# Kernel optimization log

Measured on AMD Instinct MI355X. Metric: run time of the kernel, lower is better.

The kernel has to match this reference:

```python
import jax, jax.numpy as jnp
from jax import lax
import numpy as np

B, CIN, HC, K, REC = 64, 64, 64, 3, 5
MG = 240 // REC  # 48
EPS = 1e-8


def conv2d(x, w, b, pad):
    y = lax.conv_general_dilated(x, w, (1, 1), [(pad, pad), (pad, pad)],
                                 dimension_numbers=('NCHW', 'OIHW', 'NCHW'))
    return y + b[None, :, None, None]


def conv_transpose2d(x, w, b, stride, pad):
    # PyTorch ConvTranspose2d: w is (Cin, Cout, kH, kW)
    k = w.shape[2]
    w_t = jnp.transpose(w[:, :, ::-1, ::-1], (1, 0, 2, 3))  # -> OIHW, flipped
    y = lax.conv_general_dilated(x, w_t, (1, 1),
                                 [(k - 1 - pad, k - 1 - pad)] * 2,
                                 lhs_dilation=(stride, stride),
                                 dimension_numbers=('NCHW', 'OIHW', 'NCHW'))
    return y + b[None, :, None, None]


def leaky(x):
    return jnp.where(x >= 0, x, 0.2 * x)


def setup_inputs() -> dict:
    key = jax.random.key(0)
    ks = jax.random.split(key, 12)
    s = 0.05
    return {
        'x': jax.random.normal(ks[0], (B, CIN, 64, 64), jnp.float32),
        'h': jax.random.normal(ks[1], (B, HC, 64, 64), jnp.float32),
        'c': jax.random.normal(ks[2], (B, HC, 64, 64), jnp.float32),
        'recalled_memory_feature': jax.random.normal(ks[3], (B, REC, MG, 32, 32), jnp.float32),
        'conv_w': jax.random.normal(ks[4], (5 * HC, CIN + HC, K, K), jnp.float32) * s,
        'conv_b': jax.random.normal(ks[5], (5 * HC,), jnp.float32) * s,
        'convc_w': jax.random.normal(ks[6], (MG, HC, 1, 1), jnp.float32) * s,
        'convc_b': jax.random.normal(ks[7], (MG,), jnp.float32) * s,
        'convssm_w': jax.random.normal(ks[8], (MG, MG, 4, 4), jnp.float32) * s,
        'convssm_b': jax.random.normal(ks[9], (MG,), jnp.float32) * s,
        'convfuse_w': jax.random.normal(ks[10], (HC, MG + HC, 1, 1), jnp.float32) * s,
        'convfuse_b': jax.random.normal(ks[11], (HC,), jnp.float32) * s,
    }


def reference(x, h, c, recalled_memory_feature, conv_w, conv_b, convc_w, convc_b,
              convssm_w, convssm_b, convfuse_w, convfuse_b):
    rm = recalled_memory_feature.reshape(B, REC, MG, 32, 32)
    rm_avg = rm.mean(axis=(3, 4))                      # (B, REC, MG)
    q = leaky(conv2d(c, convc_w, convc_b, 0))          # (B, MG, 64, 64)
    q_avg = q.mean(axis=(2, 3))                        # (B, MG)
    # cosine similarity along channel dim, vectorized over (B, REC)
    qn = jnp.maximum(jnp.linalg.norm(q_avg, axis=1, keepdims=True), EPS)   # (B,1)
    mn = jnp.maximum(jnp.linalg.norm(rm_avg, axis=2), EPS)                  # (B,REC)
    cos = jnp.einsum('bm,brm->br', q_avg, rm_avg) / (qn * mn)               # (B,REC)
    attn = jax.nn.softmax(cos, axis=1)                                      # (B,REC)
    mt = jnp.einsum('br,brmhw->bmhw', attn, rm)        # (B, MG, 32, 32)
    mt = leaky(conv_transpose2d(mt, convssm_w, convssm_b, 2, 1))  # (B, MG, 64, 64)

    gates = conv2d(jnp.concatenate((x, h), axis=1), conv_w, conv_b, K // 2)
    i, f, g, o, lam = jnp.split(gates, 5, axis=1)
    i = jax.nn.sigmoid(i)
    f = jax.nn.sigmoid(f)
    o = jax.nn.sigmoid(o)
    g = jnp.tanh(g)
    lam = jax.nn.sigmoid(lam)
    c_new = f * c + i * g
    h_new = o * jnp.tanh(conv2d(jnp.concatenate((c_new, mt), axis=1), convfuse_w, convfuse_b, 0))
    h_out = lam * h_new + (1.0 - lam) * h
    return (h_out, c_new)
```

## Files before the change

### kernel.cpp

```cpp
#include <hip/hip_runtime.h>
#include <hip/hip_bf16.h>
#include <cstdint>

#define HW 4096
#define MGc 48
#define RECc 5

typedef __attribute__((ext_vector_type(8))) short bf16x8;
typedef __attribute__((ext_vector_type(4))) float f32x4;

__device__ __forceinline__ float sigf(float x) { return 1.f / (1.f + expf(-x)); }
__device__ __forceinline__ float leakyf(float x) { return x >= 0.f ? x : 0.2f * x; }
__device__ __forceinline__ unsigned short f2bfu(float f) {
  __hip_bfloat16 b = __float2bfloat16(f);
  return *reinterpret_cast<unsigned short*>(&b);
}
__device__ __forceinline__ void gload_lds16(const void* g, void* l) {
  __builtin_amdgcn_global_load_lds(
      (const __attribute__((address_space(1))) unsigned int*)g,
      (__attribute__((address_space(3))) unsigned int*)l, 16, 0, 0);
}

__global__ __launch_bounds__(256) void k_rm_sum(const float* __restrict__ rm,
                                                float* __restrict__ rm_sum) {
  int row = blockIdx.x;
  const float4* p = reinterpret_cast<const float4*>(rm + (size_t)row * 1024);
  float4 v = p[threadIdx.x];
  float s = v.x + v.y + v.z + v.w;
  #pragma unroll
  for (int off = 32; off; off >>= 1) s += __shfl_down(s, off);
  __shared__ float sred[4];
  if ((threadIdx.x & 63) == 0) sred[threadIdx.x >> 6] = s;
  __syncthreads();
  if (threadIdx.x == 0) rm_sum[row] = sred[0] + sred[1] + sred[2] + sred[3];
}

__global__ __launch_bounds__(256) void k_q_part(const float* __restrict__ c,
    const float* __restrict__ ccw, const float* __restrict__ ccb,
    float* __restrict__ q_part) {
  __shared__ float wl[MGc * 64];
  __shared__ float bl[MGc];
  __shared__ float red[4][MGc];
  int b = blockIdx.y, seg = blockIdx.x;
  for (int i = threadIdx.x; i < MGc * 64; i += 256) wl[i] = ccw[i];
  if (threadIdx.x < MGc) bl[threadIdx.x] = ccb[threadIdx.x];
  __syncthreads();
  int px = seg * 256 + threadIdx.x;
  float acc[MGc];
  #pragma unroll
  for (int m = 0; m < MGc; m++) acc[m] = 0.f;
  const float* cp = c + (size_t)b * 64 * HW + px;
  for (int ci = 0; ci < 64; ci++) {
    float v = cp[(size_t)ci * HW];
    #pragma unroll
    for (int m = 0; m < MGc; m++) acc[m] += wl[m * 64 + ci] * v;
  }
  int lane = threadIdx.x & 63, wv = threadIdx.x >> 6;
  #pragma unroll
  for (int m = 0; m < MGc; m++) {
    float t = leakyf(acc[m] + bl[m]);
    #pragma unroll
    for (int off = 32; off; off >>= 1) t += __shfl_down(t, off);
    if (lane == 0) red[wv][m] = t;
  }
  __syncthreads();
  if (threadIdx.x < MGc) {
    float t = red[0][threadIdx.x] + red[1][threadIdx.x] + red[2][threadIdx.x] + red[3][threadIdx.x];
    q_part[((size_t)b * 16 + seg) * MGc + threadIdx.x] = t;
  }
}

__global__ __launch_bounds__(64) void k_attn(const float* __restrict__ rm_sum,
    const float* __restrict__ q_part, float* __restrict__ attn) {
  int b = blockIdx.x, lane = threadIdx.x;
  float q = 0.f;
  if (lane < MGc) {
    float s = 0.f;
    for (int sg = 0; sg < 16; sg++) s += q_part[((size_t)b * 16 + sg) * MGc + lane];
    q = s * (1.f / 4096.f);
  }
  float qs = q * q;
  #pragma unroll
  for (int off = 32; off; off >>= 1) qs += __shfl_xor(qs, off);
  float qn = fmaxf(sqrtf(qs), 1e-8f);
  float cosv[RECc];
  #pragma unroll
  for (int r = 0; r < RECc; r++) {
    float m = 0.f;
    if (lane < MGc) m = rm_sum[((size_t)b * RECc + r) * MGc + lane] * (1.f / 1024.f);
    float d = q * m, ms = m * m;
    #pragma unroll
    for (int off = 32; off; off >>= 1) { d += __shfl_xor(d, off); ms += __shfl_xor(ms, off); }
    float mn = fmaxf(sqrtf(ms), 1e-8f);
    cosv[r] = d / (qn * mn);
  }
  float mx = cosv[0];
  #pragma unroll
  for (int r = 1; r < RECc; r++) mx = fmaxf(mx, cosv[r]);
  float ssum = 0.f;
  #pragma unroll
  for (int r = 0; r < RECc; r++) { cosv[r] = expf(cosv[r] - mx); ssum += cosv[r]; }
  float inv = 1.f / ssum;
  #pragma unroll
  for (int r = 0; r < RECc; r++)
    if (lane == r) attn[b * RECc + r] = cosv[r] * inv;
}

__global__ __launch_bounds__(256) void k_mt_pre(const float* __restrict__ rm,
    const float* __restrict__ attn, float* __restrict__ mt_pre) {
  int idx = blockIdx.x * 256 + threadIdx.x;
  int b = idx / (MGc * 1024);
  int rem = idx - b * (MGc * 1024);
  const float* ap = attn + b * RECc;
  const float* base = rm + (size_t)b * RECc * MGc * 1024 + rem;
  float v = ap[0] * base[0] + ap[1] * base[MGc * 1024] + ap[2] * base[2 * MGc * 1024]
          + ap[3] * base[3 * MGc * 1024] + ap[4] * base[4 * MGc * 1024];
  mt_pre[idx] = v;
}

__global__ __launch_bounds__(512) void k_ssm(const float* __restrict__ mt_pre,
    const float* __restrict__ w, const float* __restrict__ bias,
    __hip_bfloat16* __restrict__ mt) {
  __shared__ float in_t[12][10][20];
  __shared__ float w_t[12][48][16];
  int b = blockIdx.y;
  int tile = blockIdx.x;
  int y0 = (tile >> 1) * 16, x0 = (tile & 1) * 32;
  int wv = threadIdx.x >> 6, lane = threadIdx.x & 63;
  int co0 = wv * 6;
  int oyl = lane >> 2, xseg = lane & 3;
  int oy = y0 + oyl;
  int iy0 = (y0 >> 1) - 1, ix0 = (x0 >> 1) - 1;
  int kyA = (oy + 1) & 1;
  int iyA = (oy + 1 - kyA) >> 1;
  int rA = iyA - iy0, rB = rA - 1;
  float acc[6][8] = {};
  for (int ch = 0; ch < 4; ch++) {
    int ci0 = ch * 12;
    __syncthreads();
    for (int i = threadIdx.x; i < 12 * 10 * 18; i += 512) {
      int ci = i / 180, rr = (i % 180) / 18, cc2 = i % 18;
      int giy = iy0 + rr, gix = ix0 + cc2;
      float v = 0.f;
      if ((unsigned)giy < 32u && (unsigned)gix < 32u)
        v = mt_pre[(((size_t)b * MGc + ci0 + ci) * 32 + giy) * 32 + gix];
      in_t[ci][rr][cc2] = v;
    }
    for (int i = threadIdx.x; i < 12 * 48 * 16; i += 512)
      (&w_t[0][0][0])[i] = w[ci0 * 768 + i];
    __syncthreads();
    #pragma unroll 1
    for (int ci = 0; ci < 12; ci++) {
      float4 a0 = *reinterpret_cast<const float4*>(&in_t[ci][rA][xseg * 4]);
      float4 a1 = *reinterpret_cast<const float4*>(&in_t[ci][rA][xseg * 4 + 4]);
      float4 b0 = *reinterpret_cast<const float4*>(&in_t[ci][rB][xseg * 4]);
      float4 b1 = *reinterpret_cast<const float4*>(&in_t[ci][rB][xseg * 4 + 4]);
      float vA[6] = {a0.x, a0.y, a0.z, a0.w, a1.x, a1.y};
      float vB[6] = {b0.x, b0.y, b0.z, b0.w, b1.x, b1.y};
      #pragma unroll
      for (int co = 0; co < 6; co++) {
        const float* wp = &w_t[ci][co0 + co][0];
        float4 wA = *reinterpret_cast<const float4*>(wp + kyA * 4);
        float4 wB = *reinterpret_cast<const float4*>(wp + (kyA + 2) * 4);
        #pragma unroll
        for (int j = 0; j < 8; j++) {
          if ((j & 1) == 0) {
            int hi = (j >> 1) + 1, lo = j >> 1;
            acc[co][j] += vA[hi] * wA.y + vA[lo] * wA.w + vB[hi] * wB.y + vB[lo] * wB.w;
          } else {
            int hi = ((j + 1) >> 1) + 1, lo = (j + 1) >> 1;
            acc[co][j] += vA[hi] * wA.x + vA[lo] * wA.z + vB[hi] * wB.x + vB[lo] * wB.z;
          }
        }
      }
    }
  }
  int oxb = x0 + xseg * 8;
  #pragma unroll
  for (int co = 0; co < 6; co++) {
    float bb = bias[co0 + co];
    size_t obase = (((size_t)b * MGc + co0 + co) * 64 + oy) * 64 + oxb;
    #pragma unroll
    for (int j = 0; j < 8; j++)
      mt[obase + j] = __float2bfloat16(leakyf(acc[co][j] + bb));
  }
}

__global__ __launch_bounds__(256) void k_ppack(const float* __restrict__ xin,
    const float* __restrict__ hin, __hip_bfloat16* __restrict__ P) {
  __shared__ float t[64][65];
  int b = blockIdx.z, y = blockIdx.y, half = blockIdx.x;
  const float* src = (half ? hin : xin) + (size_t)b * 64 * HW + y * 64;
  #pragma unroll
  for (int it = 0; it < 4; it++) {
    int li = it * 256 + threadIdx.x;
    int ci = li >> 4, x4 = (li & 15) * 4;
    float4 v = *reinterpret_cast<const float4*>(src + (size_t)ci * HW + x4);
    t[x4][ci] = v.x; t[x4 + 1][ci] = v.y; t[x4 + 2][ci] = v.z; t[x4 + 3][ci] = v.w;
  }
  __syncthreads();
  int x = threadIdx.x >> 2, c16 = (threadIdx.x & 3) * 16;
  unsigned short* dst = reinterpret_cast<unsigned short*>(P) +
      (((size_t)b * 4096 + (size_t)y * 64 + x) * 128 + half * 64 + c16);
  bf16x8 o0, o1;
  #pragma unroll
  for (int j = 0; j < 8; j++) {
    o0[j] = (short)f2bfu(t[x][c16 + j]);
    o1[j] = (short)f2bfu(t[x][c16 + 8 + j]);
  }
  *reinterpret_cast<bf16x8*>(dst) = o0;
  *reinterpret_cast<bf16x8*>(dst + 8) = o1;
}

__global__ __launch_bounds__(256) void k_wpack(const float* __restrict__ cw,
                                               __hip_bfloat16* __restrict__ Wp) {
  int idx = blockIdx.x * 256 + threadIdx.x;
  if (idx >= 9 * 320 * 128) return;
  int t = idx / (320 * 128);
  int rem = idx % (320 * 128);
  int ocp = rem / 128, ci = rem % 128;
  int nt = ocp / 80, r2 = ocp % 80, gate = r2 / 16, ml = r2 % 16;
  int oc = gate * 64 + nt * 16 + ml;
  float v = cw[((size_t)oc * 128 + ci) * 9 + t];
  Wp[idx] = __float2bfloat16(v);
}

__global__ __launch_bounds__(512) void k_gates_mfma(
    const __hip_bfloat16* __restrict__ P, const __hip_bfloat16* __restrict__ Wp,
    const float* __restrict__ c, const float* __restrict__ cb,
    float* __restrict__ c_new, __hip_bfloat16* __restrict__ o_g,
    __hip_bfloat16* __restrict__ lam_g) {
  __shared__ bf16x8 s_in[18 * 4 * 66];
  __shared__ bf16x8 s_w[9 * 4 * 80];
  int b = blockIdx.y;
  int ytile = blockIdx.x >> 2, nt = blockIdx.x & 3;
  int y0 = ytile * 16;
  int tid = threadIdx.x;
  int wv = tid >> 6, lane = tid & 63;
  int wr = wv >> 2, xw = wv & 3;
  int lane15 = lane & 15, lq = lane >> 4;

  f32x4 acc[8][5];
  #pragma unroll
  for (int i = 0; i < 8; i++)
    #pragma unroll
    for (int j = 0; j < 5; j++) acc[i][j] = (f32x4)0.f;

  const char* Pb = (const char*)P;
  const char* Wb = (const char*)Wp;

  for (int cc = 0; cc < 4; cc++) {
    __syncthreads();
    #pragma unroll 1
    for (int u = wv; u < 72; u += 8) {
      int L = u >> 2, g = u & 3;
      int y = y0 - 1 + L;
      bf16x8* dst = &s_in[u * 66];
      if ((unsigned)y < 64u) {
        const char* gp = Pb + ((((size_t)b * 4096 + (size_t)y * 64 + lane) * 128) + cc * 32 + g * 8) * 2;
        gload_lds16(gp, (void*)(dst + 1));
        if (lane < 2) dst[lane * 65] = (bf16x8)0;
      } else {
        dst[lane] = (bf16x8)0;
        if (lane < 2) dst[64 + lane] = (bf16x8)0;
      }
    }
    #pragma unroll 1
    for (int u = wv; u < 45; u += 8) {
      int e = u * 64 + lane;
      int t = e / 320, rem = e % 320;
      int g = rem / 80, ol = rem % 80;
      const char* gp = Wb + (((size_t)t * 320 + nt * 80 + ol) * 128 + cc * 32 + g * 8) * 2;
      gload_lds16(gp, (void*)&s_w[e]);
    }
    __syncthreads();

    #pragma unroll
    for (int dx = 0; dx < 3; dx++) {
      bf16x8 af[10];
      #pragma unroll
      for (int ri = 0; ri < 10; ri++) {
        int L = wr * 8 + ri;
        af[ri] = s_in[(L * 4 + lq) * 66 + (xw * 16 + lane15 + dx)];
      }
      #pragma unroll
      for (int ky = 0; ky < 3; ky++) {
        int t = ky * 3 + dx;
        bf16x8 bw[5];
        #pragma unroll
        for (int gg = 0; gg < 5; gg++)
          bw[gg] = s_w[(t * 4 + lq) * 80 + gg * 16 + lane15];
        #pragma unroll
        for (int rr = 0; rr < 8; rr++) {
          #pragma unroll
          for (int gg = 0; gg < 5; gg++)
            acc[rr][gg] = __builtin_amdgcn_mfma_f32_16x16x32_bf16(
                af[rr + ky], bw[gg], acc[rr][gg], 0, 0, 0);
        }
      }
    }
  }

  int m_hid = nt * 16 + lane15;
  float bi = cb[m_hid], bff = cb[64 + m_hid], bgg = cb[128 + m_hid],
        bo = cb[192 + m_hid], bl = cb[256 + m_hid];
  int xb = xw * 16 + lq * 4;
  size_t chofs = ((size_t)b * 64 + m_hid) * HW;
  #pragma unroll
  for (int rr = 0; rr < 8; rr++) {
    int y = y0 + wr * 8 + rr;
    size_t pofs = chofs + (size_t)y * 64 + xb;
    f32x4 cold = *reinterpret_cast<const f32x4*>(c + pofs);
    f32x4 cn;
    unsigned short ov[4], lv[4];
    #pragma unroll
    for (int e = 0; e < 4; e++) {
      float i_ = sigf(acc[rr][0][e] + bi);
      float f_ = sigf(acc[rr][1][e] + bff);
      float g_ = tanhf(acc[rr][2][e] + bgg);
      float o_ = sigf(acc[rr][3][e] + bo);
      float l_ = sigf(acc[rr][4][e] + bl);
      cn[e] = f_ * cold[e] + i_ * g_;
      ov[e] = f2bfu(o_);
      lv[e] = f2bfu(l_);
    }
    *reinterpret_cast<f32x4*>(c_new + pofs) = cn;
    ushort4 ovv = {ov[0], ov[1], ov[2], ov[3]};
    ushort4 lvv = {lv[0], lv[1], lv[2], lv[3]};
    *reinterpret_cast<ushort4*>(reinterpret_cast<unsigned short*>(o_g) + pofs) = ovv;
    *reinterpret_cast<ushort4*>(reinterpret_cast<unsigned short*>(lam_g) + pofs) = lvv;
  }
}

__global__ __launch_bounds__(256) void k_fuse(const float* __restrict__ c_new,
    const __hip_bfloat16* __restrict__ mt, const __hip_bfloat16* __restrict__ o_g,
    const __hip_bfloat16* __restrict__ lam_g, const float* __restrict__ h,
    const float* __restrict__ fw, const float* __restrict__ fb,
    float* __restrict__ h_out) {
  __shared__ float wl[112][64];
  int b = blockIdx.y, seg = blockIdx.x;
  for (int i = threadIdx.x; i < 112 * 64; i += 256) {
    int ci = i >> 6, co = i & 63;
    wl[ci][co] = fw[co * 112 + ci];
  }
  __syncthreads();
  int px = seg * 256 + threadIdx.x;
  size_t bofs = (size_t)b * 64 * HW;
  float acc[64];
  #pragma unroll
  for (int co = 0; co < 64; co++) acc[co] = fb[co];
  #pragma unroll 1
  for (int ci = 0; ci < 64; ci++) {
    float v = c_new[bofs + (size_t)ci * HW + px];
    #pragma unroll
    for (int c4 = 0; c4 < 16; c4++) {
      float4 w = *reinterpret_cast<const float4*>(&wl[ci][c4 * 4]);
      acc[c4 * 4 + 0] += w.x * v; acc[c4 * 4 + 1] += w.y * v;
      acc[c4 * 4 + 2] += w.z * v; acc[c4 * 4 + 3] += w.w * v;
    }
  }
  size_t mtofs = (size_t)b * MGc * HW + px;
  #pragma unroll 1
  for (int ci = 0; ci < 48; ci++) {
    float v = __bfloat162float(mt[mtofs + (size_t)ci * HW]);
    #pragma unroll
    for (int c4 = 0; c4 < 16; c4++) {
      float4 w = *reinterpret_cast<const float4*>(&wl[64 + ci][c4 * 4]);
      acc[c4 * 4 + 0] += w.x * v; acc[c4 * 4 + 1] += w.y * v;
      acc[c4 * 4 + 2] += w.z * v; acc[c4 * 4 + 3] += w.w * v;
    }
  }
  #pragma unroll
  for (int co = 0; co < 64; co++) {
    size_t ofs = bofs + (size_t)co * HW + px;
    float hn = tanhf(acc[co]);
    float ov = __bfloat162float(o_g[ofs]);
    float lv = __bfloat162float(lam_g[ofs]);
    float hv = h[ofs];
    h_out[ofs] = lv * (ov * hn) + (1.f - lv) * hv;
  }
}

extern "C" void kernel_launch(void* const* d_in, const int* in_sizes, int n_in,
                              void* d_out, int out_size, void* d_ws, size_t ws_size,
                              hipStream_t stream) {
  const float* x   = (const float*)d_in[0];
  const float* h   = (const float*)d_in[1];
  const float* c   = (const float*)d_in[2];
  const float* rm  = (const float*)d_in[3];
  const float* cw  = (const float*)d_in[4];
  const float* cb  = (const float*)d_in[5];
  const float* ccw = (const float*)d_in[6];
  const float* ccb = (const float*)d_in[7];
  const float* sw  = (const float*)d_in[8];
  const float* sb  = (const float*)d_in[9];
  const float* fw  = (const float*)d_in[10];
  const float* fb  = (const float*)d_in[11];

  float* h_out = (float*)d_out;
  float* c_new = h_out + (size_t)16777216;

  char* ws = (char*)d_ws;
  float* rm_sum = (float*)(ws + 0);
  float* q_part = (float*)(ws + 65536);
  float* attn   = (float*)(ws + 262144);
  float* mt_pre = (float*)(ws + 327680);
  __hip_bfloat16* mt    = (__hip_bfloat16*)(ws + 12910592);
  __hip_bfloat16* o_g   = (__hip_bfloat16*)(ws + 38076416);
  __hip_bfloat16* lam_g = (__hip_bfloat16*)(ws + 71630848);
  __hip_bfloat16* P     = (__hip_bfloat16*)(ws + 105185280);
  __hip_bfloat16* Wp    = (__hip_bfloat16*)(ws + 172294144);

  k_wpack<<<1440, 256, 0, stream>>>(cw, Wp);
  k_ppack<<<dim3(2, 64, 64), 256, 0, stream>>>(x, h, P);
  k_rm_sum<<<15360, 256, 0, stream>>>(rm, rm_sum);
  k_q_part<<<dim3(16, 64), 256, 0, stream>>>(c, ccw, ccb, q_part);
  k_attn<<<64, 64, 0, stream>>>(rm_sum, q_part, attn);
  k_mt_pre<<<12288, 256, 0, stream>>>(rm, attn, mt_pre);
  k_ssm<<<dim3(8, 64), 512, 0, stream>>>(mt_pre, sw, sb, mt);
  k_gates_mfma<<<dim3(16, 64), 512, 0, stream>>>(P, Wp, c, cb, c_new, o_g, lam_g);
  k_fuse<<<dim3(16, 64), 256, 0, stream>>>(c_new, mt, o_g, lam_g, h, fw, fb, h_out);
}
```

Measured before the change: 717.2 us.

## Fuse attention into mt_pre, remap gates blocks, and widen fuse to two pixels per thread

Three separate changes. The k_attn kernel is removed and every k_mt_pre block now recomputes its batch's softmax attention weights into shared memory, which saves a launch but repeats that small computation in each of the 12288 blocks. k_gates_mfma remaps its block index so that consecutive blocks are spread across batches, probably to improve cache or XCD locality for the shared weights. k_fuse now handles two pixels per thread with float2 and packed bf16 loads, halving the grid and reusing each LDS weight read across two pixels, at the cost of twice as many accumulator registers.

```diff
diff --git a/kernel.cpp b/kernel.cpp
--- a/kernel.cpp
+++ b/kernel.cpp
@@ -14,6 +14,10 @@
 __device__ __forceinline__ unsigned short f2bfu(float f) {
   __hip_bfloat16 b = __float2bfloat16(f);
   return *reinterpret_cast<unsigned short*>(&b);
+}
+__device__ __forceinline__ float bfu2f(unsigned short u) {
+  unsigned v = ((unsigned)u) << 16;
+  return __uint_as_float(v);
 }
 __device__ __forceinline__ void gload_lds16(const void* g, void* l) {
   __builtin_amdgcn_global_load_lds(
@@ -70,51 +74,51 @@
   }
 }
 
-__global__ __launch_bounds__(64) void k_attn(const float* __restrict__ rm_sum,
-    const float* __restrict__ q_part, float* __restrict__ attn) {
-  int b = blockIdx.x, lane = threadIdx.x;
-  float q = 0.f;
-  if (lane < MGc) {
-    float s = 0.f;
-    for (int sg = 0; sg < 16; sg++) s += q_part[((size_t)b * 16 + sg) * MGc + lane];
-    q = s * (1.f / 4096.f);
-  }
-  float qs = q * q;
-  #pragma unroll
-  for (int off = 32; off; off >>= 1) qs += __shfl_xor(qs, off);
-  float qn = fmaxf(sqrtf(qs), 1e-8f);
-  float cosv[RECc];
-  #pragma unroll
-  for (int r = 0; r < RECc; r++) {
-    float m = 0.f;
-    if (lane < MGc) m = rm_sum[((size_t)b * RECc + r) * MGc + lane] * (1.f / 1024.f);
-    float d = q * m, ms = m * m;
-    #pragma unroll
-    for (int off = 32; off; off >>= 1) { d += __shfl_xor(d, off); ms += __shfl_xor(ms, off); }
-    float mn = fmaxf(sqrtf(ms), 1e-8f);
-    cosv[r] = d / (qn * mn);
-  }
-  float mx = cosv[0];
-  #pragma unroll
-  for (int r = 1; r < RECc; r++) mx = fmaxf(mx, cosv[r]);
-  float ssum = 0.f;
-  #pragma unroll
-  for (int r = 0; r < RECc; r++) { cosv[r] = expf(cosv[r] - mx); ssum += cosv[r]; }
-  float inv = 1.f / ssum;
-  #pragma unroll
-  for (int r = 0; r < RECc; r++)
-    if (lane == r) attn[b * RECc + r] = cosv[r] * inv;
-}
-
 __global__ __launch_bounds__(256) void k_mt_pre(const float* __restrict__ rm,
-    const float* __restrict__ attn, float* __restrict__ mt_pre) {
+    const float* __restrict__ rm_sum, const float* __restrict__ q_part,
+    float* __restrict__ mt_pre) {
+  __shared__ float sat[RECc];
   int idx = blockIdx.x * 256 + threadIdx.x;
   int b = idx / (MGc * 1024);
+  if (threadIdx.x < 64) {
+    int lane = threadIdx.x;
+    float q = 0.f;
+    if (lane < MGc) {
+      float s = 0.f;
+      for (int sg = 0; sg < 16; sg++) s += q_part[((size_t)b * 16 + sg) * MGc + lane];
+      q = s * (1.f / 4096.f);
+    }
+    float qs = q * q;
+    #pragma unroll
+    for (int off = 32; off; off >>= 1) qs += __shfl_xor(qs, off);
+    float qn = fmaxf(sqrtf(qs), 1e-8f);
+    float cosv[RECc];
+    #pragma unroll
+    for (int r = 0; r < RECc; r++) {
+      float m = 0.f;
+      if (lane < MGc) m = rm_sum[((size_t)b * RECc + r) * MGc + lane] * (1.f / 1024.f);
+      float d = q * m, ms = m * m;
+      #pragma unroll
+      for (int off = 32; off; off >>= 1) { d += __shfl_xor(d, off); ms += __shfl_xor(ms, off); }
+      float mn = fmaxf(sqrtf(ms), 1e-8f);
+      cosv[r] = d / (qn * mn);
+    }
+    float mx = cosv[0];
+    #pragma unroll
+    for (int r = 1; r < RECc; r++) mx = fmaxf(mx, cosv[r]);
+    float ssum = 0.f;
+    #pragma unroll
+    for (int r = 0; r < RECc; r++) { cosv[r] = expf(cosv[r] - mx); ssum += cosv[r]; }
+    float inv = 1.f / ssum;
+    #pragma unroll
+    for (int r = 0; r < RECc; r++)
+      if (lane == r) sat[r] = cosv[r] * inv;
+  }
+  __syncthreads();
   int rem = idx - b * (MGc * 1024);
-  const float* ap = attn + b * RECc;
   const float* base = rm + (size_t)b * RECc * MGc * 1024 + rem;
-  float v = ap[0] * base[0] + ap[1] * base[MGc * 1024] + ap[2] * base[2 * MGc * 1024]
-          + ap[3] * base[3 * MGc * 1024] + ap[4] * base[4 * MGc * 1024];
+  float v = sat[0] * base[0] + sat[1] * base[MGc * 1024] + sat[2] * base[2 * MGc * 1024]
+          + sat[3] * base[3 * MGc * 1024] + sat[4] * base[4 * MGc * 1024];
   mt_pre[idx] = v;
 }
 
@@ -232,8 +236,10 @@
     __hip_bfloat16* __restrict__ lam_g) {
   __shared__ bf16x8 s_in[18 * 4 * 66];
   __shared__ bf16x8 s_w[9 * 4 * 80];
-  int b = blockIdx.y;
-  int ytile = blockIdx.x >> 2, nt = blockIdx.x & 3;
+  int orig = blockIdx.y * gridDim.x + blockIdx.x;
+  int t_id = (orig & 7) * 128 + (orig >> 3);
+  int b = t_id >> 4;
+  int ytile = (t_id >> 2) & 3, nt = t_id & 3;
   int y0 = ytile * 16;
   int tid = threadIdx.x;
   int wv = tid >> 6, lane = tid & 63;
@@ -344,40 +350,54 @@
     wl[ci][co] = fw[co * 112 + ci];
   }
   __syncthreads();
-  int px = seg * 256 + threadIdx.x;
+  int px = seg * 512 + threadIdx.x * 2;
   size_t bofs = (size_t)b * 64 * HW;
-  float acc[64];
-  #pragma unroll
-  for (int co = 0; co < 64; co++) acc[co] = fb[co];
+  float2 acc[64];
+  #pragma unroll
+  for (int co = 0; co < 64; co++) { float bv = fb[co]; acc[co].x = bv; acc[co].y = bv; }
   #pragma unroll 1
   for (int ci = 0; ci < 64; ci++) {
-    float v = c_new[bofs + (size_t)ci * HW + px];
+    float2 v = *reinterpret_cast<const float2*>(c_new + bofs + (size_t)ci * HW + px);
     #pragma unroll
     for (int c4 = 0; c4 < 16; c4++) {
       float4 w = *reinterpret_cast<const float4*>(&wl[ci][c4 * 4]);
-      acc[c4 * 4 + 0] += w.x * v; acc[c4 * 4 + 1] += w.y * v;
-      acc[c4 * 4 + 2] += w.z * v; acc[c4 * 4 + 3] += w.w * v;
-    }
-  }
+      acc[c4 * 4 + 0].x += w.x * v.x; acc[c4 * 4 + 0].y += w.x * v.y;
+      acc[c4 * 4 + 1].x += w.y * v.x; acc[c4 * 4 + 1].y += w.y * v.y;
+      acc[c4 * 4 + 2].x += w.z * v.x; acc[c4 * 4 + 2].y += w.z * v.y;
+      acc[c4 * 4 + 3].x += w.w * v.x; acc[c4 * 4 + 3].y += w.w * v.y;
+    }
+  }
+  const unsigned short* mtu = reinterpret_cast<const unsigned short*>(mt);
   size_t mtofs = (size_t)b * MGc * HW + px;
   #pragma unroll 1
   for (int ci = 0; ci < 48; ci++) {
-    float v = __bfloat162float(mt[mtofs + (size_t)ci * HW]);
+    unsigned u = *reinterpret_cast<const unsigned*>(mtu + mtofs + (size_t)ci * HW);
+    float vx = bfu2f((unsigned short)(u & 0xffff));
+    float vy = bfu2f((unsigned short)(u >> 16));
     #pragma unroll
     for (int c4 = 0; c4 < 16; c4++) {
       float4 w = *reinterpret_cast<const float4*>(&wl[64 + ci][c4 * 4]);
-      acc[c4 * 4 + 0] += w.x * v; acc[c4 * 4 + 1] += w.y * v;
-      acc[c4 * 4 + 2] += w.z * v; acc[c4 * 4 + 3] += w.w * v;
-    }
-  }
+      acc[c4 * 4 + 0].x += w.x * vx; acc[c4 * 4 + 0].y += w.x * vy;
+      acc[c4 * 4 + 1].x += w.y * vx; acc[c4 * 4 + 1].y += w.y * vy;
+      acc[c4 * 4 + 2].x += w.z * vx; acc[c4 * 4 + 2].y += w.z * vy;
+      acc[c4 * 4 + 3].x += w.w * vx; acc[c4 * 4 + 3].y += w.w * vy;
+    }
+  }
+  const unsigned short* ou = reinterpret_cast<const unsigned short*>(o_g);
+  const unsigned short* lu = reinterpret_cast<const unsigned short*>(lam_g);
   #pragma unroll
   for (int co = 0; co < 64; co++) {
     size_t ofs = bofs + (size_t)co * HW + px;
-    float hn = tanhf(acc[co]);
-    float ov = __bfloat162float(o_g[ofs]);
-    float lv = __bfloat162float(lam_g[ofs]);
-    float hv = h[ofs];
-    h_out[ofs] = lv * (ov * hn) + (1.f - lv) * hv;
+    unsigned uo = *reinterpret_cast<const unsigned*>(ou + ofs);
+    unsigned ul = *reinterpret_cast<const unsigned*>(lu + ofs);
+    float2 hv = *reinterpret_cast<const float2*>(h + ofs);
+    float hnx = tanhf(acc[co].x), hny = tanhf(acc[co].y);
+    float ox = bfu2f((unsigned short)(uo & 0xffff)), oy = bfu2f((unsigned short)(uo >> 16));
+    float lx = bfu2f((unsigned short)(ul & 0xffff)), ly = bfu2f((unsigned short)(ul >> 16));
+    float2 r;
+    r.x = lx * (ox * hnx) + (1.f - lx) * hv.x;
+    r.y = ly * (oy * hny) + (1.f - ly) * hv.y;
+    *reinterpret_cast<float2*>(h_out + ofs) = r;
   }
 }
 
@@ -403,7 +423,6 @@
   char* ws = (char*)d_ws;
   float* rm_sum = (float*)(ws + 0);
   float* q_part = (float*)(ws + 65536);
-  float* attn   = (float*)(ws + 262144);
   float* mt_pre = (float*)(ws + 327680);
   __hip_bfloat16* mt    = (__hip_bfloat16*)(ws + 12910592);
   __hip_bfloat16* o_g   = (__hip_bfloat16*)(ws + 38076416);
@@ -415,9 +434,8 @@
   k_ppack<<<dim3(2, 64, 64), 256, 0, stream>>>(x, h, P);
   k_rm_sum<<<15360, 256, 0, stream>>>(rm, rm_sum);
   k_q_part<<<dim3(16, 64), 256, 0, stream>>>(c, ccw, ccb, q_part);
-  k_attn<<<64, 64, 0, stream>>>(rm_sum, q_part, attn);
-  k_mt_pre<<<12288, 256, 0, stream>>>(rm, attn, mt_pre);
+  k_mt_pre<<<12288, 256, 0, stream>>>(rm, rm_sum, q_part, mt_pre);
   k_ssm<<<dim3(8, 64), 512, 0, stream>>>(mt_pre, sw, sb, mt);
   k_gates_mfma<<<dim3(16, 64), 512, 0, stream>>>(P, Wp, c, cb, c_new, o_g, lam_g);
-  k_fuse<<<dim3(16, 64), 256, 0, stream>>>(c_new, mt, o_g, lam_g, h, fw, fb, h_out);
-}
+  k_fuse<<<dim3(8, 64), 256, 0, stream>>>(c_new, mt, o_g, lam_g, h, fw, fb, h_out);
+}
```

After: 691.7 us. 3.6% less time.
